# Kernel optimization log

Measured on AMD Instinct MI355X. Metric: run time of the kernel, lower is better.

Reference implementation:

```python
import jax, jax.numpy as jnp
import numpy as np
import math

LMAX = 2
MUL = 8        # output_size (mul_in1 == mul_in2)
MUL_OUT = 32   # channels_out == hidden_dim_conv
NB = 10        # number_of_basis
MAX_RADIUS = 5.0
N_NODES = 10000
N_EDGES = 320000
N_GRAPHS = 16


def _w3j(j1, j2, j3, m1, m2, m3):
    if m1 + m2 + m3 != 0:
        return 0.0
    if not (abs(j1 - j2) <= j3 <= j1 + j2):
        return 0.0
    if abs(m1) > j1 or abs(m2) > j2 or abs(m3) > j3:
        return 0.0
    f = math.factorial
    t1, t2 = j2 - m1 - j3, j1 + m2 - j3
    t3, t4, t5 = j1 + j2 - j3, j1 - m1, j2 + m2
    s = 0.0
    for t in range(max(0, t1, t2), min(t3, t4, t5) + 1):
        s += (-1) ** t / (f(t) * f(t - t1) * f(t - t2) * f(t3 - t) * f(t4 - t) * f(t5 - t))
    tri = math.sqrt(f(j1 + j2 - j3) * f(j1 - j2 + j3) * f(-j1 + j2 + j3) / f(j1 + j2 + j3 + 1))
    s *= tri * math.sqrt(f(j1 + m1) * f(j1 - m1) * f(j2 + m2) * f(j2 - m2) * f(j3 + m3) * f(j3 - m3))
    return s * (-1) ** (j1 - j2 - m3)


def _real_U(l):
    # complex->real spherical harmonic change of basis; rows real m', cols complex m (both -l..l)
    U = np.zeros((2 * l + 1, 2 * l + 1), dtype=np.complex128)
    U[l, l] = 1.0
    for m in range(1, l + 1):
        U[l + m, l + m] = (-1) ** m / math.sqrt(2)
        U[l + m, l - m] = 1 / math.sqrt(2)
        U[l - m, l - m] = 1j / math.sqrt(2)
        U[l - m, l + m] = -1j * (-1) ** m / math.sqrt(2)
    return U


def _real_cg(l1, l2, l3):
    C = np.zeros((2 * l1 + 1, 2 * l2 + 1, 2 * l3 + 1), dtype=np.complex128)
    for m1 in range(-l1, l1 + 1):
        for m2 in range(-l2, l2 + 1):
            m3 = m1 + m2
            if abs(m3) > l3:
                continue
            cg = (-1) ** (-l1 + l2 - m3) * math.sqrt(2 * l3 + 1) * _w3j(l1, l2, l3, m1, m2, -m3)
            C[m1 + l1, m2 + l2, m3 + l3] = cg
    U1, U2, U3 = _real_U(l1), _real_U(l2), _real_U(l3)
    R = np.einsum('am,bn,co,mno->abc', U1, U2, U3.conj(), C)
    return np.real(R) if np.abs(R.real).sum() >= np.abs(R.imag).sum() else np.imag(R)


PATHS = [(l1, l2, l3) for l1 in range(LMAX + 1) for l2 in range(LMAX + 1)
         for l3 in range(abs(l1 - l2), min(l1 + l2, LMAX) + 1)]  # 15 paths for lmax=2
CG = {p: jnp.asarray(_real_cg(*p), dtype=jnp.float32) for p in PATHS}
NUM_PATHS = len(PATHS)


def _harmonics(n):
    # component-normalized real direction harmonics l=0,1,2 of unit vectors n (E,3)
    x, y, z = n[:, 0], n[:, 1], n[:, 2]
    Y0 = jnp.ones_like(x)[:, None]
    Y1 = math.sqrt(3.0) * n
    a = math.sqrt(15.0)
    Y2 = jnp.stack([a * x * y, a * y * z, (math.sqrt(5.0) / 2) * (3 * z * z - 1),
                    a * x * z, (a / 2) * (x * x - y * y)], axis=-1)
    return [Y0, Y1, Y2]


def _radial_basis(r):
    # soft_one_hot_linspace, gaussian basis, cutoff=True, then * sqrt(NB)
    values = jnp.linspace(0.0, MAX_RADIUS, NB + 2)[1:-1]
    step = MAX_RADIUS / (NB + 1)
    d = (r[:, None] - values) / step
    return (jnp.exp(-d * d) / 1.12) * math.sqrt(NB)


def setup_inputs() -> dict:
    key = jax.random.key(0)
    ks = jax.random.split(key, 20)
    inp = {}
    inp['pos'] = jax.random.normal(ks[0], (N_NODES, 3), jnp.float32) * 3.0
    inp['edge_shifts'] = jnp.zeros((N_EDGES, 3), jnp.float32)
    inp['cell'] = jax.random.normal(ks[1], (N_GRAPHS, 3, 3), jnp.float32)
    inp['atom_emb'] = jax.random.normal(ks[2], (10, 16), jnp.float32)
    inp['mlp_w1'] = jax.random.normal(ks[3], (16, 64), jnp.float32) / 4.0
    inp['mlp_b1'] = jax.random.normal(ks[4], (64,), jnp.float32) * 0.1
    inp['mlp_w2'] = jax.random.normal(ks[5], (64, 8), jnp.float32) / 8.0
    inp['mlp_b2'] = jax.random.normal(ks[6], (8,), jnp.float32) * 0.1
    inp['fc_w1'] = jax.random.normal(ks[7], (NB, 64), jnp.float32) / math.sqrt(NB)
    inp['fc_b1'] = jax.random.normal(ks[8], (64,), jnp.float32) * 0.1
    inp['fc_w2'] = jax.random.normal(ks[9], (64, 64), jnp.float32) / 8.0
    inp['fc_b2'] = jax.random.normal(ks[10], (64,), jnp.float32) * 0.1
    inp['fc_w3'] = jax.random.normal(ks[11], (64, NUM_PATHS), jnp.float32) / 8.0
    inp['fc_b3'] = jax.random.normal(ks[12], (NUM_PATHS,), jnp.float32) * 0.1
    inp['tp_w'] = jax.random.normal(ks[13], (NUM_PATHS, MUL, MUL, MUL_OUT), jnp.float32) / 8.0
    inp['A'] = jax.random.randint(ks[14], (N_NODES,), 0, 10, jnp.int32)
    inp['batch'] = jnp.sort(jax.random.randint(ks[15], (N_NODES,), 0, N_GRAPHS, jnp.int32))
    inp['edge_src'] = jax.random.randint(ks[16], (N_EDGES,), 0, N_NODES, jnp.int32)
    inp['edge_dst'] = jax.random.randint(ks[17], (N_EDGES,), 0, N_NODES, jnp.int32)
    return inp


def reference(pos, edge_shifts, cell, atom_emb, mlp_w1, mlp_b1, mlp_w2, mlp_b2,
              fc_w1, fc_b1, fc_w2, fc_b2, fc_w3, fc_b3, tp_w,
              A, batch, edge_src, edge_dst):
    E = edge_src.shape[0]
    # edge geometry: gather + PBC shift
    shift = jnp.einsum('ei,eij->ej', edge_shifts, cell[batch[edge_src]])
    edge_vec = pos[edge_dst] - pos[edge_src] + shift
    edge_len = jnp.linalg.norm(edge_vec, axis=1)
    n = edge_vec / jnp.maximum(edge_len, 1e-8)[:, None]
    # atom scalars Ai: Embedding -> Linear/SiLU/Linear -> (N, MUL)
    h = jax.nn.silu(atom_emb[A] @ mlp_w1 + mlp_b1)
    Ai = h @ mlp_w2 + mlp_b2
    # per-edge irreps inputs: f_in[l] = Ai[src] outer Y_l(n); x2 only l=0 (rest are zeros)
    Y = _harmonics(n)
    Ai_src = Ai[edge_src]
    f_in = [Ai_src[:, :, None] * Y[l][:, None, :] for l in range(LMAX + 1)]
    x2_0 = Ai[edge_dst][:, :, None]  # (E, MUL, 1)
    # per-edge path gates from radial basis
    g = jax.nn.silu(_radial_basis(edge_len) @ fc_w1 + fc_b1)
    g = jax.nn.silu(g @ fc_w2 + fc_b2)
    gates = g @ fc_w3 + fc_b3  # (E, NUM_PATHS)
    # fully-connected CG tensor product; paths with l2>0 contract zero blocks -> skipped
    out_blocks = [jnp.zeros((E, MUL_OUT, 2 * l + 1), Ai.dtype) for l in range(LMAX + 1)]
    for p, (l1, l2, l3) in enumerate(PATHS):
        if l2 > 0:
            continue
        msg = jnp.einsum('eui,evj,uvw,ijk->ewk', f_in[l1], x2_0, tp_w[p], CG[(l1, l2, l3)])
        out_blocks[l3] = out_blocks[l3] + gates[:, p][:, None, None] * msg
    edge_feat = jnp.concatenate([b.reshape(E, -1) for b in out_blocks], axis=-1)  # (E, 288)
    # mean-aggregate over destination nodes
    ones = jnp.ones((E,), edge_feat.dtype)
    cnt = jnp.maximum(jax.ops.segment_sum(ones, edge_dst, num_segments=N_NODES), 1.0)
    out = jax.ops.segment_sum(edge_feat, edge_dst, num_segments=N_NODES) / cnt[:, None]
    return out
```

## Files before the change

kernel.cpp:

```cpp
#include <hip/hip_runtime.h>
#include <math.h>

#define N_NODES 10000
#define N_EDGES 320000
#define CAP 128
#define TN 8192
#define TSCALE 1024.0f
#define AI_BLOCKS 40
#define TB_BLOCKS 2049

__device__ __forceinline__ float silu_f(float x) {
    return x / (1.0f + __expf(-x));
}

__global__ __launch_bounds__(256) void prep_kernel(
    const float* __restrict__ atom_emb, const int* __restrict__ A,
    const float* __restrict__ w1, const float* __restrict__ b1,
    const float* __restrict__ w2, const float* __restrict__ b2,
    const float* __restrict__ fw1, const float* __restrict__ fb1,
    const float* __restrict__ fw2, const float* __restrict__ fb2,
    const float* __restrict__ fw3, const float* __restrict__ fb3,
    float* __restrict__ Ai, float4* __restrict__ tab, int* __restrict__ deg)
{
    int bid = blockIdx.x;
    if (bid < AI_BLOCKS) {
        int n = bid * 256 + threadIdx.x;
        if (n >= N_NODES) return;
        deg[n] = 0;
        int a = A[n];
        float emb[16];
        #pragma unroll
        for (int i = 0; i < 16; ++i) emb[i] = atom_emb[a * 16 + i];
        float acc[8];
        #pragma unroll
        for (int o = 0; o < 8; ++o) acc[o] = b2[o];
        #pragma unroll 4
        for (int j = 0; j < 64; ++j) {
            float s0 = b1[j], s1 = 0.f;
            #pragma unroll
            for (int i = 0; i < 16; i += 2) {
                s0 += emb[i]     * w1[i * 64 + j];
                s1 += emb[i + 1] * w1[(i + 1) * 64 + j];
            }
            float h = silu_f(s0 + s1);
            #pragma unroll
            for (int o = 0; o < 8; ++o) acc[o] += h * w2[j * 8 + o];
        }
        #pragma unroll
        for (int o = 0; o < 8; ++o) Ai[n * 8 + o] = acc[o];
        return;
    }

    int lane = threadIdx.x & 63;
    int t = (bid - AI_BLOCKS) * 4 + (threadIdx.x >> 6);
    if (t > TN) return;
    float r = (float)t * (1.0f / TSCALE);

    float rb[10];
    {
        float x = r * 2.2f;
        #pragma unroll
        for (int i = 0; i < 10; ++i) {
            float d = x - (float)(i + 1);
            rb[i] = __expf(-d * d) * 2.8234622f;
        }
    }

    float g1;
    {
        float s = fb1[lane];
        #pragma unroll
        for (int k = 0; k < 10; ++k) s += rb[k] * fw1[k * 64 + lane];
        g1 = silu_f(s);
    }

    float acc = fb2[lane];
    #pragma unroll 8
    for (int i = 0; i < 64; ++i) {
        float gi = __shfl(g1, i, 64);
        acc += gi * fw2[i * 64 + lane];
    }
    float h = silu_f(acc);

    float p0 = h * fw3[lane * 15 + 0];
    float p3 = h * fw3[lane * 15 + 3];
    float p9 = h * fw3[lane * 15 + 9];
    #pragma unroll
    for (int m = 1; m < 64; m <<= 1) {
        p0 += __shfl_xor(p0, m, 64);
        p3 += __shfl_xor(p3, m, 64);
        p9 += __shfl_xor(p9, m, 64);
    }
    if (lane == 0) {
        tab[t] = make_float4(fb3[0] + p0, fb3[3] + p3, fb3[9] + p9, 0.f);
    }
}

__global__ __launch_bounds__(256) void bucket_kernel(
    const int* __restrict__ edge_src, const int* __restrict__ edge_dst,
    const float* __restrict__ pos, const float* __restrict__ edge_shifts,
    const float* __restrict__ cell, const int* __restrict__ batch,
    int* __restrict__ deg, float4* __restrict__ elist)
{
    int e = blockIdx.x * 256 + threadIdx.x;
    int dst = edge_dst[e];
    int src = edge_src[e];

    float s0 = edge_shifts[e * 3 + 0];
    float s1 = edge_shifts[e * 3 + 1];
    float s2 = edge_shifts[e * 3 + 2];

    float vx = pos[dst * 3 + 0] - pos[src * 3 + 0];
    float vy = pos[dst * 3 + 1] - pos[src * 3 + 1];
    float vz = pos[dst * 3 + 2] - pos[src * 3 + 2];

    if (s0 != 0.f || s1 != 0.f || s2 != 0.f) {
        int b = batch[src];
        const float* Cb = cell + b * 9;
        vx += s0 * Cb[0] + s1 * Cb[3] + s2 * Cb[6];
        vy += s0 * Cb[1] + s1 * Cb[4] + s2 * Cb[7];
        vz += s0 * Cb[2] + s1 * Cb[5] + s2 * Cb[8];
    }

    int p = atomicAdd(&deg[dst], 1);
    if (p < CAP) {
        elist[dst * CAP + p] = make_float4(vx, vy, vz, __int_as_float(src));
    }
}

__global__ __launch_bounds__(256) void gather_out_kernel(
    const int* __restrict__ deg, const float4* __restrict__ elist,
    const float4* __restrict__ tab, const float* __restrict__ Ai,
    const float* __restrict__ tp_w, float* __restrict__ out)
{
    __shared__ float sM[4][72];
    __shared__ float sA[4][8];
    int tid = threadIdx.x;
    int lane = tid & 63;
    int wv = tid >> 6;
    int nodeBase = blockIdx.x * 4;
    int n1 = nodeBase + wv;
    int u1 = lane & 7;
    int slot = lane >> 3;

    int d = deg[n1];
    int dc = d > CAP ? CAP : d;

    const float SQ3 = 1.7320508075688772f;
    const float SQ15 = 3.872983346207417f;
    const float SQ5H = 1.1180339887498949f;

    float acc[9];
    #pragma unroll
    for (int k = 0; k < 9; ++k) acc[k] = 0.f;

    const float4* el = elist + n1 * CAP;
    for (int i = slot; i < dc; i += 8) {
        float4 rec = el[i];
        float vx = rec.x, vy = rec.y, vz = rec.z;
        int src = __float_as_int(rec.w);

        float r = sqrtf(vx * vx + vy * vy + vz * vz);
        float rinv = 1.0f / fmaxf(r, 1e-8f);
        float nx = vx * rinv, ny = vy * rinv, nz = vz * rinv;

        float tf = fminf(r * TSCALE, (float)(TN - 1));
        int   i0 = (int)tf;
        float fr = tf - (float)i0;
        float4 ga = tab[i0];
        float4 gb = tab[i0 + 1];
        float gate0 = ga.x + fr * (gb.x - ga.x);
        float gate3 = ga.y + fr * (gb.y - ga.y);
        float gate9 = ga.z + fr * (gb.z - ga.z);

        float au = Ai[src * 8 + u1];

        acc[0] += gate0 * au;
        float g3a = gate3 * au;
        acc[1] += g3a * (SQ3 * nx);
        acc[2] += g3a * (SQ3 * ny);
        acc[3] += g3a * (SQ3 * nz);
        float g9a = gate9 * au;
        acc[4] += g9a * (SQ15 * nx * ny);
        acc[5] += g9a * (SQ15 * ny * nz);
        acc[6] += g9a * (SQ5H * (3.0f * nz * nz - 1.0f));
        acc[7] += g9a * (SQ15 * nx * nz);
        acc[8] += g9a * (0.5f * SQ15 * (nx * nx - ny * ny));
    }

    #pragma unroll
    for (int m = 8; m < 64; m <<= 1) {
        #pragma unroll
        for (int k = 0; k < 9; ++k) acc[k] += __shfl_xor(acc[k], m, 64);
    }

    if (slot == 0) {
        #pragma unroll
        for (int k = 0; k < 9; ++k) sM[wv][u1 * 9 + k] = acc[k];
    }
    if (tid < 32) sA[tid >> 3][tid & 7] = Ai[nodeBase * 8 + tid];
    __syncthreads();

    if (tid >= 128) return;
    int ln = tid >> 5, w = tid & 31;
    int n = nodeBase + ln;

    float a[8];
    #pragma unroll
    for (int v = 0; v < 8; ++v) a[v] = sA[ln][v];
    float inv = 1.0f / fmaxf((float)deg[n], 1.0f);

    const float* W0 = tp_w + 0 * 2048;
    const float* W3 = tp_w + 3 * 2048;
    const float* W9 = tp_w + 9 * 2048;

    {
        float o0 = 0.f;
        #pragma unroll
        for (int u = 0; u < 8; ++u) {
            float c = 0.f;
            #pragma unroll
            for (int v = 0; v < 8; ++v) c += a[v] * W0[(u * 8 + v) * 32 + w];
            o0 += sM[ln][u * 9] * c;
        }
        out[n * 288 + w] = o0 * inv;
    }
    {
        float o1[3] = {0.f, 0.f, 0.f};
        #pragma unroll
        for (int u = 0; u < 8; ++u) {
            float c = 0.f;
            #pragma unroll
            for (int v = 0; v < 8; ++v) c += a[v] * W3[(u * 8 + v) * 32 + w];
            #pragma unroll
            for (int k = 0; k < 3; ++k) o1[k] += sM[ln][u * 9 + 1 + k] * c;
        }
        #pragma unroll
        for (int k = 0; k < 3; ++k) out[n * 288 + 32 + w * 3 + k] = o1[k] * inv;
    }
    {
        float o2[5] = {0.f, 0.f, 0.f, 0.f, 0.f};
        #pragma unroll
        for (int u = 0; u < 8; ++u) {
            float c = 0.f;
            #pragma unroll
            for (int v = 0; v < 8; ++v) c += a[v] * W9[(u * 8 + v) * 32 + w];
            #pragma unroll
            for (int k = 0; k < 5; ++k) o2[k] += sM[ln][u * 9 + 4 + k] * c;
        }
        #pragma unroll
        for (int k = 0; k < 5; ++k) out[n * 288 + 128 + w * 5 + k] = o2[k] * inv;
    }
}

extern "C" void kernel_launch(void* const* d_in, const int* in_sizes, int n_in,
                              void* d_out, int out_size, void* d_ws, size_t ws_size,
                              hipStream_t stream) {
    const float* pos         = (const float*)d_in[0];
    const float* edge_shifts = (const float*)d_in[1];
    const float* cell        = (const float*)d_in[2];
    const float* atom_emb    = (const float*)d_in[3];
    const float* mlp_w1      = (const float*)d_in[4];
    const float* mlp_b1      = (const float*)d_in[5];
    const float* mlp_w2      = (const float*)d_in[6];
    const float* mlp_b2      = (const float*)d_in[7];
    const float* fc_w1       = (const float*)d_in[8];
    const float* fc_b1       = (const float*)d_in[9];
    const float* fc_w2       = (const float*)d_in[10];
    const float* fc_b2       = (const float*)d_in[11];
    const float* fc_w3       = (const float*)d_in[12];
    const float* fc_b3       = (const float*)d_in[13];
    const float* tp_w        = (const float*)d_in[14];
    const int*   A           = (const int*)d_in[15];
    const int*   batch       = (const int*)d_in[16];
    const int*   edge_src    = (const int*)d_in[17];
    const int*   edge_dst    = (const int*)d_in[18];
    float* out = (float*)d_out;

    float4* elist = (float4*)d_ws;
    float*  Ai    = (float*)(elist + (size_t)N_NODES * CAP);
    float4* tab   = (float4*)(Ai + N_NODES * 8);
    int*    deg   = (int*)(tab + (TN + 1));

    prep_kernel<<<AI_BLOCKS + TB_BLOCKS, 256, 0, stream>>>(
        atom_emb, A, mlp_w1, mlp_b1, mlp_w2, mlp_b2,
        fc_w1, fc_b1, fc_w2, fc_b2, fc_w3, fc_b3, Ai, tab, deg);

    bucket_kernel<<<N_EDGES / 256, 256, 0, stream>>>(
        edge_src, edge_dst, pos, edge_shifts, cell, batch, deg, elist);

    gather_out_kernel<<<N_NODES / 4, 256, 0, stream>>>(
        deg, elist, tab, Ai, tp_w, out);
}
```

Measured before the change: 156.0 us.

## Fuse edge bucketing with prep kernel and unroll gather loop by two

Merges the edge-bucketing kernel into the prep kernel, so edge bucketing, the gate-table MLP and the node embedding MLP run as independent block ranges of one launch. The degree array is now zeroed with a memset beforehand, because bucketing no longer depends on prep. Each bucketing thread handles two edges. The gather loop is unrolled to issue two edge-record loads per iteration, and the shared-memory Ai load is hoisted earlier. The aim is to cut a kernel launch and the serialization between prep and bucketing, and to expose more memory-level parallelism, at the cost of an extra memset call.

```diff
diff --git a/kernel.cpp b/kernel.cpp
--- a/kernel.cpp
+++ b/kernel.cpp
@@ -6,126 +6,120 @@
 #define CAP 128
 #define TN 8192
 #define TSCALE 1024.0f
+#define BK_BLOCKS 625
+#define TB_BLOCKS 2049
 #define AI_BLOCKS 40
-#define TB_BLOCKS 2049
 
 __device__ __forceinline__ float silu_f(float x) {
     return x / (1.0f + __expf(-x));
 }
 
-__global__ __launch_bounds__(256) void prep_kernel(
+__global__ __launch_bounds__(256) void fused_prep_kernel(
+    const int* __restrict__ edge_src, const int* __restrict__ edge_dst,
+    const float* __restrict__ pos, const float* __restrict__ edge_shifts,
+    const float* __restrict__ cell, const int* __restrict__ batch,
     const float* __restrict__ atom_emb, const int* __restrict__ A,
     const float* __restrict__ w1, const float* __restrict__ b1,
     const float* __restrict__ w2, const float* __restrict__ b2,
     const float* __restrict__ fw1, const float* __restrict__ fb1,
     const float* __restrict__ fw2, const float* __restrict__ fb2,
     const float* __restrict__ fw3, const float* __restrict__ fb3,
-    float* __restrict__ Ai, float4* __restrict__ tab, int* __restrict__ deg)
+    float* __restrict__ Ai, float4* __restrict__ tab,
+    int* __restrict__ deg, float4* __restrict__ elist)
 {
     int bid = blockIdx.x;
-    if (bid < AI_BLOCKS) {
-        int n = bid * 256 + threadIdx.x;
-        if (n >= N_NODES) return;
-        deg[n] = 0;
-        int a = A[n];
-        float emb[16];
-        #pragma unroll
-        for (int i = 0; i < 16; ++i) emb[i] = atom_emb[a * 16 + i];
-        float acc[8];
-        #pragma unroll
-        for (int o = 0; o < 8; ++o) acc[o] = b2[o];
-        #pragma unroll 4
-        for (int j = 0; j < 64; ++j) {
-            float s0 = b1[j], s1 = 0.f;
-            #pragma unroll
-            for (int i = 0; i < 16; i += 2) {
-                s0 += emb[i]     * w1[i * 64 + j];
-                s1 += emb[i + 1] * w1[(i + 1) * 64 + j];
+    if (bid < BK_BLOCKS) {
+        int e1 = bid * 256 + threadIdx.x;
+        int e2 = e1 + (N_EDGES / 2);
+        #pragma unroll
+        for (int pass = 0; pass < 2; ++pass) {
+            int e = pass ? e2 : e1;
+            int dst = edge_dst[e];
+            int src = edge_src[e];
+            float s0 = edge_shifts[e * 3 + 0];
+            float s1 = edge_shifts[e * 3 + 1];
+            float s2 = edge_shifts[e * 3 + 2];
+            float vx = pos[dst * 3 + 0] - pos[src * 3 + 0];
+            float vy = pos[dst * 3 + 1] - pos[src * 3 + 1];
+            float vz = pos[dst * 3 + 2] - pos[src * 3 + 2];
+            if (s0 != 0.f || s1 != 0.f || s2 != 0.f) {
+                int b = batch[src];
+                const float* Cb = cell + b * 9;
+                vx += s0 * Cb[0] + s1 * Cb[3] + s2 * Cb[6];
+                vy += s0 * Cb[1] + s1 * Cb[4] + s2 * Cb[7];
+                vz += s0 * Cb[2] + s1 * Cb[5] + s2 * Cb[8];
             }
-            float h = silu_f(s0 + s1);
-            #pragma unroll
-            for (int o = 0; o < 8; ++o) acc[o] += h * w2[j * 8 + o];
-        }
-        #pragma unroll
-        for (int o = 0; o < 8; ++o) Ai[n * 8 + o] = acc[o];
+            int p = atomicAdd(&deg[dst], 1);
+            if (p < CAP) elist[dst * CAP + p] = make_float4(vx, vy, vz, __int_as_float(src));
+        }
         return;
     }
-
-    int lane = threadIdx.x & 63;
-    int t = (bid - AI_BLOCKS) * 4 + (threadIdx.x >> 6);
-    if (t > TN) return;
-    float r = (float)t * (1.0f / TSCALE);
-
-    float rb[10];
-    {
-        float x = r * 2.2f;
-        #pragma unroll
-        for (int i = 0; i < 10; ++i) {
-            float d = x - (float)(i + 1);
-            rb[i] = __expf(-d * d) * 2.8234622f;
-        }
-    }
-
-    float g1;
-    {
-        float s = fb1[lane];
-        #pragma unroll
-        for (int k = 0; k < 10; ++k) s += rb[k] * fw1[k * 64 + lane];
-        g1 = silu_f(s);
-    }
-
-    float acc = fb2[lane];
-    #pragma unroll 8
-    for (int i = 0; i < 64; ++i) {
-        float gi = __shfl(g1, i, 64);
-        acc += gi * fw2[i * 64 + lane];
-    }
-    float h = silu_f(acc);
-
-    float p0 = h * fw3[lane * 15 + 0];
-    float p3 = h * fw3[lane * 15 + 3];
-    float p9 = h * fw3[lane * 15 + 9];
-    #pragma unroll
-    for (int m = 1; m < 64; m <<= 1) {
-        p0 += __shfl_xor(p0, m, 64);
-        p3 += __shfl_xor(p3, m, 64);
-        p9 += __shfl_xor(p9, m, 64);
-    }
-    if (lane == 0) {
-        tab[t] = make_float4(fb3[0] + p0, fb3[3] + p3, fb3[9] + p9, 0.f);
-    }
-}
-
-__global__ __launch_bounds__(256) void bucket_kernel(
-    const int* __restrict__ edge_src, const int* __restrict__ edge_dst,
-    const float* __restrict__ pos, const float* __restrict__ edge_shifts,
-    const float* __restrict__ cell, const int* __restrict__ batch,
-    int* __restrict__ deg, float4* __restrict__ elist)
-{
-    int e = blockIdx.x * 256 + threadIdx.x;
-    int dst = edge_dst[e];
-    int src = edge_src[e];
-
-    float s0 = edge_shifts[e * 3 + 0];
-    float s1 = edge_shifts[e * 3 + 1];
-    float s2 = edge_shifts[e * 3 + 2];
-
-    float vx = pos[dst * 3 + 0] - pos[src * 3 + 0];
-    float vy = pos[dst * 3 + 1] - pos[src * 3 + 1];
-    float vz = pos[dst * 3 + 2] - pos[src * 3 + 2];
-
-    if (s0 != 0.f || s1 != 0.f || s2 != 0.f) {
-        int b = batch[src];
-        const float* Cb = cell + b * 9;
-        vx += s0 * Cb[0] + s1 * Cb[3] + s2 * Cb[6];
-        vy += s0 * Cb[1] + s1 * Cb[4] + s2 * Cb[7];
-        vz += s0 * Cb[2] + s1 * Cb[5] + s2 * Cb[8];
-    }
-
-    int p = atomicAdd(&deg[dst], 1);
-    if (p < CAP) {
-        elist[dst * CAP + p] = make_float4(vx, vy, vz, __int_as_float(src));
-    }
+    if (bid < BK_BLOCKS + TB_BLOCKS) {
+        int lane = threadIdx.x & 63;
+        int t = (bid - BK_BLOCKS) * 4 + (threadIdx.x >> 6);
+        if (t > TN) return;
+        float r = (float)t * (1.0f / TSCALE);
+
+        float rb[10];
+        {
+            float x = r * 2.2f;
+            #pragma unroll
+            for (int i = 0; i < 10; ++i) {
+                float d = x - (float)(i + 1);
+                rb[i] = __expf(-d * d) * 2.8234622f;
+            }
+        }
+        float g1;
+        {
+            float s = fb1[lane];
+            #pragma unroll
+            for (int k = 0; k < 10; ++k) s += rb[k] * fw1[k * 64 + lane];
+            g1 = silu_f(s);
+        }
+        float acc = fb2[lane];
+        #pragma unroll 8
+        for (int i = 0; i < 64; ++i) {
+            float gi = __shfl(g1, i, 64);
+            acc += gi * fw2[i * 64 + lane];
+        }
+        float h = silu_f(acc);
+
+        float p0 = h * fw3[lane * 15 + 0];
+        float p3 = h * fw3[lane * 15 + 3];
+        float p9 = h * fw3[lane * 15 + 9];
+        #pragma unroll
+        for (int m = 1; m < 64; m <<= 1) {
+            p0 += __shfl_xor(p0, m, 64);
+            p3 += __shfl_xor(p3, m, 64);
+            p9 += __shfl_xor(p9, m, 64);
+        }
+        if (lane == 0) tab[t] = make_float4(fb3[0] + p0, fb3[3] + p3, fb3[9] + p9, 0.f);
+        return;
+    }
+
+    int n = (bid - BK_BLOCKS - TB_BLOCKS) * 256 + threadIdx.x;
+    if (n >= N_NODES) return;
+    int a = A[n];
+    float emb[16];
+    #pragma unroll
+    for (int i = 0; i < 16; ++i) emb[i] = atom_emb[a * 16 + i];
+    float acc[8];
+    #pragma unroll
+    for (int o = 0; o < 8; ++o) acc[o] = b2[o];
+    #pragma unroll 4
+    for (int j = 0; j < 64; ++j) {
+        float s0 = b1[j], s1 = 0.f;
+        #pragma unroll
+        for (int i = 0; i < 16; i += 2) {
+            s0 += emb[i]     * w1[i * 64 + j];
+            s1 += emb[i + 1] * w1[(i + 1) * 64 + j];
+        }
+        float h = silu_f(s0 + s1);
+        #pragma unroll
+        for (int o = 0; o < 8; ++o) acc[o] += h * w2[j * 8 + o];
+    }
+    #pragma unroll
+    for (int o = 0; o < 8; ++o) Ai[n * 8 + o] = acc[o];
 }
 
 __global__ __launch_bounds__(256) void gather_out_kernel(
@@ -143,6 +137,8 @@
     int u1 = lane & 7;
     int slot = lane >> 3;
 
+    if (tid < 32) sA[tid >> 3][tid & 7] = Ai[nodeBase * 8 + tid];
+
     int d = deg[n1];
     int dc = d > CAP ? CAP : d;
 
@@ -155,38 +151,47 @@
     for (int k = 0; k < 9; ++k) acc[k] = 0.f;
 
     const float4* el = elist + n1 * CAP;
-    for (int i = slot; i < dc; i += 8) {
-        float4 rec = el[i];
-        float vx = rec.x, vy = rec.y, vz = rec.z;
-        int src = __float_as_int(rec.w);
-
-        float r = sqrtf(vx * vx + vy * vy + vz * vz);
-        float rinv = 1.0f / fmaxf(r, 1e-8f);
-        float nx = vx * rinv, ny = vy * rinv, nz = vz * rinv;
-
-        float tf = fminf(r * TSCALE, (float)(TN - 1));
-        int   i0 = (int)tf;
-        float fr = tf - (float)i0;
-        float4 ga = tab[i0];
-        float4 gb = tab[i0 + 1];
-        float gate0 = ga.x + fr * (gb.x - ga.x);
-        float gate3 = ga.y + fr * (gb.y - ga.y);
-        float gate9 = ga.z + fr * (gb.z - ga.z);
-
-        float au = Ai[src * 8 + u1];
-
-        acc[0] += gate0 * au;
-        float g3a = gate3 * au;
-        acc[1] += g3a * (SQ3 * nx);
-        acc[2] += g3a * (SQ3 * ny);
-        acc[3] += g3a * (SQ3 * nz);
-        float g9a = gate9 * au;
-        acc[4] += g9a * (SQ15 * nx * ny);
-        acc[5] += g9a * (SQ15 * ny * nz);
-        acc[6] += g9a * (SQ5H * (3.0f * nz * nz - 1.0f));
-        acc[7] += g9a * (SQ15 * nx * nz);
-        acc[8] += g9a * (0.5f * SQ15 * (nx * nx - ny * ny));
-    }
+
+#define PROC(rec) do {                                                   \
+        float vx = (rec).x, vy = (rec).y, vz = (rec).z;                  \
+        int src = __float_as_int((rec).w);                               \
+        float rr = sqrtf(vx * vx + vy * vy + vz * vz);                   \
+        float rinv = 1.0f / fmaxf(rr, 1e-8f);                            \
+        float nx = vx * rinv, ny = vy * rinv, nz = vz * rinv;            \
+        float tf = fminf(rr * TSCALE, (float)(TN - 1));                  \
+        int   i0 = (int)tf;                                              \
+        float fr = tf - (float)i0;                                       \
+        float4 ga = tab[i0];                                             \
+        float4 gb = tab[i0 + 1];                                         \
+        float gate0 = ga.x + fr * (gb.x - ga.x);                         \
+        float gate3 = ga.y + fr * (gb.y - ga.y);                         \
+        float gate9 = ga.z + fr * (gb.z - ga.z);                         \
+        float au = Ai[src * 8 + u1];                                     \
+        acc[0] += gate0 * au;                                            \
+        float g3a = gate3 * au;                                          \
+        acc[1] += g3a * (SQ3 * nx);                                      \
+        acc[2] += g3a * (SQ3 * ny);                                      \
+        acc[3] += g3a * (SQ3 * nz);                                      \
+        float g9a = gate9 * au;                                          \
+        acc[4] += g9a * (SQ15 * nx * ny);                                \
+        acc[5] += g9a * (SQ15 * ny * nz);                                \
+        acc[6] += g9a * (SQ5H * (3.0f * nz * nz - 1.0f));                \
+        acc[7] += g9a * (SQ15 * nx * nz);                                \
+        acc[8] += g9a * (0.5f * SQ15 * (nx * nx - ny * ny));             \
+    } while (0)
+
+    int i = slot;
+    for (; i + 8 < dc; i += 16) {
+        float4 r1 = el[i];
+        float4 r2 = el[i + 8];
+        PROC(r1);
+        PROC(r2);
+    }
+    if (i < dc) {
+        float4 r1 = el[i];
+        PROC(r1);
+    }
+#undef PROC
 
     #pragma unroll
     for (int m = 8; m < 64; m <<= 1) {
@@ -198,7 +203,6 @@
         #pragma unroll
         for (int k = 0; k < 9; ++k) sM[wv][u1 * 9 + k] = acc[k];
     }
-    if (tid < 32) sA[tid >> 3][tid & 7] = Ai[nodeBase * 8 + tid];
     __syncthreads();
 
     if (tid >= 128) return;
@@ -282,12 +286,12 @@
     float4* tab   = (float4*)(Ai + N_NODES * 8);
     int*    deg   = (int*)(tab + (TN + 1));
 
-    prep_kernel<<<AI_BLOCKS + TB_BLOCKS, 256, 0, stream>>>(
+    hipMemsetAsync(deg, 0, N_NODES * sizeof(int), stream);
+
+    fused_prep_kernel<<<BK_BLOCKS + TB_BLOCKS + AI_BLOCKS, 256, 0, stream>>>(
+        edge_src, edge_dst, pos, edge_shifts, cell, batch,
         atom_emb, A, mlp_w1, mlp_b1, mlp_w2, mlp_b2,
-        fc_w1, fc_b1, fc_w2, fc_b2, fc_w3, fc_b3, Ai, tab, deg);
-
-    bucket_kernel<<<N_EDGES / 256, 256, 0, stream>>>(
-        edge_src, edge_dst, pos, edge_shifts, cell, batch, deg, elist);
+        fc_w1, fc_b1, fc_w2, fc_b2, fc_w3, fc_b3, Ai, tab, deg, elist);
 
     gather_out_kernel<<<N_NODES / 4, 256, 0, stream>>>(
         deg, elist, tab, Ai, tp_w, out);
```

Result: faster. 152.6 us (-2.2%).
